# Kernel optimization log

Hardware: AMD Instinct MI355X
Metric: run time of the kernel (lower is better)

## Reference

```python
import jax, jax.numpy as jnp
import numpy as np

ALPHA = 1.0  # module hardcodes self.alpha = 1.0


def _normalize(m):
    # torch: diag(rowsum^-0.5) @ m @ diag(rowsum^-0.5) == broadcast row/col scaling
    r_inv = jnp.sum(m, axis=0) ** -0.5  # [V]
    return m * r_inv[:, None] * r_inv[None, :]


def setup_inputs() -> dict:
    key = jax.random.key(0)
    k1, k2, k3, k4 = jax.random.split(key, 4)
    V, D_IN, D_OUT, A, B = 2048, 64, 64, 8, 8
    adj = jax.random.uniform(k1, (V, V), dtype=jnp.float32)
    x = jax.random.normal(k2, (A, B, V, D_IN), dtype=jnp.float32)
    # xavier_normal_ on [D_IN, D_OUT]
    std = float(np.sqrt(2.0 / (D_IN + D_OUT)))
    weight = jax.random.normal(k3, (D_IN, D_OUT), dtype=jnp.float32) * std
    bias = jax.random.normal(k4, (D_OUT,), dtype=jnp.float32)
    return {"adj": adj, "x": x, "weight": weight, "bias": bias}


def reference(adj, x, weight, bias):
    # dropout is identity in eval mode
    adj_norm = _normalize(adj)
    sqr_norm = _normalize(adj @ adj)  # computed as in the original (alpha=1 zeroes it)
    m_norm = ALPHA * adj_norm + (1.0 - ALPHA) * sqr_norm  # [V, V]
    x_tmp = jnp.einsum('abvd,de->abve', x, weight)        # project features
    x_out = jnp.einsum('vj,abvd->abjd', m_norm, x_tmp)    # aggregate over nodes
    x_out = x_out + bias
    return jax.nn.relu(x_out)
```

## Files before the change

kernel.cpp:

```cpp
#include <hip/hip_runtime.h>
#include <cstddef>

typedef unsigned short u16;
typedef u16 u16x4 __attribute__((ext_vector_type(4)));
typedef u16 u16x8 __attribute__((ext_vector_type(8)));
typedef __bf16 bf16x8 __attribute__((ext_vector_type(8)));
typedef float f32x4 __attribute__((ext_vector_type(4)));

static constexpr int V  = 2048;
static constexpr int DD = 64;

__device__ __forceinline__ u16 f2b(float f) {
  union { float f; unsigned int i; } x; x.f = f;
  return (u16)((x.i + 0x7fffu + ((x.i >> 16) & 1u)) >> 16);
}

__device__ __forceinline__ void gll16(const void* g, void* l) {
  __builtin_amdgcn_global_load_lds(
      (const __attribute__((address_space(1))) void*)g,
      (__attribute__((address_space(3))) void*)l, 16, 0, 0);
}

__global__ __launch_bounds__(256) void k_pp(const float* __restrict__ adj,
                                            const float* __restrict__ x,
                                            const float* __restrict__ w,
                                            float* __restrict__ partial,
                                            u16* __restrict__ Yt) {
  __shared__ u16 WT[64 * 72];
  int t = threadIdx.x;
  int bid = blockIdx.x;

  if (bid < 256) {
    int rg = bid >> 3, cg = bid & 7;
    int col = cg * 256 + t;
    const float* p = adj + (size_t)(rg * 64) * V + col;
    float s = 0.f;
    for (int r = 0; r < 64; ++r) s += p[(size_t)r * V];
    partial[(size_t)rg * V + col] = s;
  } else {
    int pb = bid - 256;
    int ab = pb >> 4;
    int v0 = (pb & 15) * 128;

    {
      const float4* pw = (const float4*)(w + t * 16);
      float4 c0 = pw[0], c1 = pw[1], c2 = pw[2], c3 = pw[3];
      float vals[16] = {c0.x, c0.y, c0.z, c0.w, c1.x, c1.y, c1.z, c1.w,
                        c2.x, c2.y, c2.z, c2.w, c3.x, c3.y, c3.z, c3.w};
      #pragma unroll
      for (int k = 0; k < 16; ++k) {
        int idx = t * 16 + k;
        WT[(idx & 63) * 72 + (idx >> 6)] = f2b(vals[k]);
      }
    }
    __syncthreads();

    int lane = t & 63, wave = t >> 6;
    int q = lane >> 4, r = lane & 15;
    int vbase = v0 + wave * 32;

    bf16x8 a[4][2];
    #pragma unroll
    for (int i = 0; i < 4; ++i)
      #pragma unroll
      for (int kk = 0; kk < 2; ++kk)
        a[i][kk] = __builtin_bit_cast(bf16x8,
            *(const u16x8*)(WT + (i * 16 + r) * 72 + kk * 32 + q * 8));

    const f32x4 vzero = {0.f, 0.f, 0.f, 0.f};
    f32x4 acc[4][2];
    #pragma unroll
    for (int i = 0; i < 4; ++i) { acc[i][0] = vzero; acc[i][1] = vzero; }

    #pragma unroll
    for (int nt = 0; nt < 2; ++nt) {
      int v = vbase + nt * 16 + r;
      const float* xp = x + ((size_t)ab * V + v) * DD;
      #pragma unroll
      for (int kk = 0; kk < 2; ++kk) {
        const float4* p = (const float4*)(xp + kk * 32 + q * 8);
        float4 b0 = p[0], b1 = p[1];
        u16x8 bu;
        bu[0] = f2b(b0.x); bu[1] = f2b(b0.y); bu[2] = f2b(b0.z); bu[3] = f2b(b0.w);
        bu[4] = f2b(b1.x); bu[5] = f2b(b1.y); bu[6] = f2b(b1.z); bu[7] = f2b(b1.w);
        bf16x8 bf = __builtin_bit_cast(bf16x8, bu);
        #pragma unroll
        for (int i = 0; i < 4; ++i)
          acc[i][nt] = __builtin_amdgcn_mfma_f32_16x16x32_bf16(bf, a[i][kk], acc[i][nt], 0, 0, 0);
      }
    }

    #pragma unroll
    for (int i = 0; i < 4; ++i) {
      int e = ab * 64 + i * 16 + r;
      #pragma unroll
      for (int nt = 0; nt < 2; ++nt) {
        int v = vbase + nt * 16 + q * 4;
        u16x4 o;
        #pragma unroll
        for (int reg = 0; reg < 4; ++reg) o[reg] = f2b(acc[i][nt][reg]);
        *(u16x4*)(Yt + (size_t)e * V + v) = o;
      }
    }
  }
}

__global__ __launch_bounds__(256) void k_tn(const float* __restrict__ adj,
                                            const float* __restrict__ partial,
                                            u16* __restrict__ At) {
  __shared__ float T[64][65];
  __shared__ float rvv[64], rvj[64];
  int t = threadIdx.x;
  int bid = blockIdx.x;
  int v0 = (bid & 31) * 64;
  int j0 = (bid >> 5) * 64;

  if (t < 128) {
    int col = (t < 64) ? (v0 + t) : (j0 + (t - 64));
    float s = 0.f;
    #pragma unroll
    for (int i = 0; i < 32; ++i) s += partial[(size_t)i * V + col];
    float rv = rsqrtf(s);
    if (t < 64) rvv[t] = rv; else rvj[t - 64] = rv;
  }
  __syncthreads();
  #pragma unroll
  for (int it = 0; it < 2; ++it) {
    int f = t + it * 256;
    int row = f >> 3;
    int cc = (f & 7) * 8;
    float rv = rvv[row];
    const float4* p = (const float4*)(adj + (size_t)(v0 + row) * V + j0 + cc);
    float4 a0 = p[0], a1 = p[1];
    T[row][cc + 0] = a0.x * rv; T[row][cc + 1] = a0.y * rv;
    T[row][cc + 2] = a0.z * rv; T[row][cc + 3] = a0.w * rv;
    T[row][cc + 4] = a1.x * rv; T[row][cc + 5] = a1.y * rv;
    T[row][cc + 6] = a1.z * rv; T[row][cc + 7] = a1.w * rv;
  }
  __syncthreads();
  #pragma unroll
  for (int it = 0; it < 2; ++it) {
    int f = t + it * 256;
    int jr = f >> 3;
    int vc = (f & 7) * 8;
    float rj = rvj[jr];
    u16x8 o;
    #pragma unroll
    for (int k = 0; k < 8; ++k) o[k] = f2b(T[vc + k][jr] * rj);
    *(u16x8*)(At + (size_t)(j0 + jr) * V + v0 + vc) = o;
  }
}

static constexpr int ABUF  = 128 * 64;
static constexpr int BUFSZ = 2 * ABUF;

__global__ __launch_bounds__(256) void k_gemm(const u16* __restrict__ At,
                                              const u16* __restrict__ Yt,
                                              const float* __restrict__ bias,
                                              float* __restrict__ out) {
  __shared__ u16 lds[2 * BUFSZ];
  const int t = threadIdx.x;
  const int bid = blockIdx.x;
  const int swz = (bid & 7) * 64 + (bid >> 3);
  const int m0 = (swz & 15) * 128;
  const int n0 = (swz >> 4) * 128;
  const int lane = t & 63, wave = t >> 6;
  const int wm = (wave & 1) * 64;
  const int wn = (wave >> 1) * 64;
  const int q = lane >> 4, r = lane & 15;

  auto stage = [&](int base, int k0) {
    #pragma unroll
    for (int l = 0; l < 4; ++l) {
      int g = l * 256 + t;
      int row = g >> 3;
      int ch = (g & 7) ^ (row & 7);
      gll16(At + (size_t)(m0 + row) * V + k0 + ch * 8, (void*)(lds + base + g * 8));
      gll16(Yt + (size_t)(n0 + row) * V + k0 + ch * 8, (void*)(lds + base + ABUF + g * 8));
    }
  };

  const f32x4 vzero = {0.f, 0.f, 0.f, 0.f};
  f32x4 acc[4][4];
  #pragma unroll
  for (int i = 0; i < 4; ++i)
    #pragma unroll
    for (int j = 0; j < 4; ++j) acc[i][j] = vzero;

  stage(0, 0);
  asm volatile("s_waitcnt vmcnt(0)" ::: "memory");
  __builtin_amdgcn_s_barrier();

  int cb = 0;
  for (int tt = 0; tt < 32; ++tt) {
    const int nb = cb ^ BUFSZ;
    if (tt < 31) stage(nb, (tt + 1) * 64);
    __builtin_amdgcn_sched_barrier(0);

    #pragma unroll
    for (int kk = 0; kk < 2; ++kk) {
      bf16x8 a[4], b[4];
      #pragma unroll
      for (int i = 0; i < 4; ++i) {
        int row = wm + i * 16 + r;
        int c = (kk * 4 + q) ^ (row & 7);
        a[i] = __builtin_bit_cast(bf16x8,
            *(const u16x8*)(lds + cb + row * 64 + c * 8));
      }
      #pragma unroll
      for (int j = 0; j < 4; ++j) {
        int row = wn + j * 16 + r;
        int c = (kk * 4 + q) ^ (row & 7);
        b[j] = __builtin_bit_cast(bf16x8,
            *(const u16x8*)(lds + cb + ABUF + row * 64 + c * 8));
      }
      __builtin_amdgcn_s_setprio(1);
      #pragma unroll
      for (int i = 0; i < 4; ++i)
        #pragma unroll
        for (int j = 0; j < 4; ++j)
          acc[i][j] = __builtin_amdgcn_mfma_f32_16x16x32_bf16(
              a[i], b[j], acc[i][j], 0, 0, 0);
      __builtin_amdgcn_s_setprio(0);
    }

    asm volatile("s_waitcnt vmcnt(0)" ::: "memory");
    __builtin_amdgcn_s_barrier();
    cb = nb;
  }

  #pragma unroll
  for (int j = 0; j < 4; ++j) {
    int n = n0 + wn + j * 16 + r;
    int e = n & 63;
    int ab = n >> 6;
    float bv = bias[e];
    float* ob = out + (size_t)ab * (V * DD);
    #pragma unroll
    for (int i = 0; i < 4; ++i) {
      #pragma unroll
      for (int reg = 0; reg < 4; ++reg) {
        int jj = m0 + wm + i * 16 + q * 4 + reg;
        ob[(size_t)jj * DD + e] = fmaxf(acc[i][j][reg] + bv, 0.f);
      }
    }
  }
}

extern "C" void kernel_launch(void* const* d_in, const int* in_sizes, int n_in,
                              void* d_out, int out_size, void* d_ws, size_t ws_size,
                              hipStream_t stream) {
  const float* adj  = (const float*)d_in[0];
  const float* x    = (const float*)d_in[1];
  const float* w    = (const float*)d_in[2];
  const float* bias = (const float*)d_in[3];
  float* out = (float*)d_out;

  char* ws = (char*)d_ws;
  u16*   At      = (u16*)ws;
  u16*   Yt      = (u16*)(ws + ((size_t)8 << 20));
  float* partial = (float*)(ws + ((size_t)24 << 20));

  k_pp<<<1280, 256, 0, stream>>>(adj, x, w, partial, Yt);
  k_tn<<<1024, 256, 0, stream>>>(adj, partial, At);
  k_gemm<<<512, 256, 0, stream>>>(At, Yt, bias, out);
}
```

Before: 143.9 us.

## Fuse three kernels into one cooperative kernel with grid syncs

Merges the column-sum/projection, transpose-normalize and GEMM kernels into a single cooperative kernel of 512 blocks, separated by grid-wide barriers. Each block now handles two work items per phase, and the column-sum partials use 64 row groups of 32 rows. The aim is to remove two kernel launch boundaries and the tail idle time between them. In exchange it adds grid-sync cost and less parallelism in the early phases, and it depends on all 512 blocks being co-resident (launch_bounds 256,2).

```diff
diff --git a/kernel.cpp b/kernel.cpp
--- a/kernel.cpp
+++ b/kernel.cpp
@@ -1,5 +1,8 @@
 #include <hip/hip_runtime.h>
+#include <hip/hip_cooperative_groups.h>
 #include <cstddef>
+
+namespace cg = cooperative_groups;
 
 typedef unsigned short u16;
 typedef u16 u16x4 __attribute__((ext_vector_type(4)));
@@ -21,27 +24,31 @@
       (__attribute__((address_space(3))) void*)l, 16, 0, 0);
 }
 
-__global__ __launch_bounds__(256) void k_pp(const float* __restrict__ adj,
-                                            const float* __restrict__ x,
-                                            const float* __restrict__ w,
-                                            float* __restrict__ partial,
-                                            u16* __restrict__ Yt) {
-  __shared__ u16 WT[64 * 72];
-  int t = threadIdx.x;
-  int bid = blockIdx.x;
-
-  if (bid < 256) {
+static constexpr int ABUF  = 128 * 64;
+static constexpr int BUFSZ = 2 * ABUF;
+
+__global__ __launch_bounds__(256, 2) void k_mega(
+    const float* __restrict__ adj, const float* __restrict__ x,
+    const float* __restrict__ w, const float* __restrict__ bias,
+    float* __restrict__ partial, u16* __restrict__ At,
+    u16* __restrict__ Yt, float* __restrict__ out) {
+  __shared__ u16 lds[2 * BUFSZ];
+  const int t = threadIdx.x;
+  const int bid = blockIdx.x;
+  const int lane = t & 63, wave = t >> 6;
+  const int q = lane >> 4, r = lane & 15;
+
+  {
     int rg = bid >> 3, cg = bid & 7;
     int col = cg * 256 + t;
-    const float* p = adj + (size_t)(rg * 64) * V + col;
+    const float* p = adj + (size_t)(rg * 32) * V + col;
     float s = 0.f;
-    for (int r = 0; r < 64; ++r) s += p[(size_t)r * V];
+    for (int rr = 0; rr < 32; ++rr) s += p[(size_t)rr * V];
     partial[(size_t)rg * V + col] = s;
-  } else {
-    int pb = bid - 256;
-    int ab = pb >> 4;
-    int v0 = (pb & 15) * 128;
-
+  }
+
+  {
+    u16* WT = lds;
     {
       const float4* pw = (const float4*)(w + t * 16);
       float4 c0 = pw[0], c1 = pw[1], c2 = pw[2], c3 = pw[3];
@@ -55,10 +62,6 @@
     }
     __syncthreads();
 
-    int lane = t & 63, wave = t >> 6;
-    int q = lane >> 4, r = lane & 15;
-    int vbase = v0 + wave * 32;
-
     bf16x8 a[4][2];
     #pragma unroll
     for (int i = 0; i < 4; ++i)
@@ -68,180 +71,186 @@
             *(const u16x8*)(WT + (i * 16 + r) * 72 + kk * 32 + q * 8));
 
     const f32x4 vzero = {0.f, 0.f, 0.f, 0.f};
-    f32x4 acc[4][2];
-    #pragma unroll
-    for (int i = 0; i < 4; ++i) { acc[i][0] = vzero; acc[i][1] = vzero; }
-
-    #pragma unroll
-    for (int nt = 0; nt < 2; ++nt) {
-      int v = vbase + nt * 16 + r;
-      const float* xp = x + ((size_t)ab * V + v) * DD;
-      #pragma unroll
-      for (int kk = 0; kk < 2; ++kk) {
-        const float4* p = (const float4*)(xp + kk * 32 + q * 8);
-        float4 b0 = p[0], b1 = p[1];
-        u16x8 bu;
-        bu[0] = f2b(b0.x); bu[1] = f2b(b0.y); bu[2] = f2b(b0.z); bu[3] = f2b(b0.w);
-        bu[4] = f2b(b1.x); bu[5] = f2b(b1.y); bu[6] = f2b(b1.z); bu[7] = f2b(b1.w);
-        bf16x8 bf = __builtin_bit_cast(bf16x8, bu);
-        #pragma unroll
-        for (int i = 0; i < 4; ++i)
-          acc[i][nt] = __builtin_amdgcn_mfma_f32_16x16x32_bf16(bf, a[i][kk], acc[i][nt], 0, 0, 0);
-      }
-    }
-
-    #pragma unroll
-    for (int i = 0; i < 4; ++i) {
-      int e = ab * 64 + i * 16 + r;
+    #pragma unroll
+    for (int sub = 0; sub < 2; ++sub) {
+      int pb = bid * 2 + sub;
+      int ab = pb >> 4;
+      int v0 = (pb & 15) * 128;
+      int vbase = v0 + wave * 32;
+
+      f32x4 acc[4][2];
+      #pragma unroll
+      for (int i = 0; i < 4; ++i) { acc[i][0] = vzero; acc[i][1] = vzero; }
+
       #pragma unroll
       for (int nt = 0; nt < 2; ++nt) {
-        int v = vbase + nt * 16 + q * 4;
-        u16x4 o;
-        #pragma unroll
-        for (int reg = 0; reg < 4; ++reg) o[reg] = f2b(acc[i][nt][reg]);
-        *(u16x4*)(Yt + (size_t)e * V + v) = o;
-      }
-    }
-  }
-}
-
-__global__ __launch_bounds__(256) void k_tn(const float* __restrict__ adj,
-                                            const float* __restrict__ partial,
-                                            u16* __restrict__ At) {
-  __shared__ float T[64][65];
-  __shared__ float rvv[64], rvj[64];
-  int t = threadIdx.x;
-  int bid = blockIdx.x;
-  int v0 = (bid & 31) * 64;
-  int j0 = (bid >> 5) * 64;
-
-  if (t < 128) {
-    int col = (t < 64) ? (v0 + t) : (j0 + (t - 64));
-    float s = 0.f;
-    #pragma unroll
-    for (int i = 0; i < 32; ++i) s += partial[(size_t)i * V + col];
-    float rv = rsqrtf(s);
-    if (t < 64) rvv[t] = rv; else rvj[t - 64] = rv;
-  }
-  __syncthreads();
-  #pragma unroll
-  for (int it = 0; it < 2; ++it) {
-    int f = t + it * 256;
-    int row = f >> 3;
-    int cc = (f & 7) * 8;
-    float rv = rvv[row];
-    const float4* p = (const float4*)(adj + (size_t)(v0 + row) * V + j0 + cc);
-    float4 a0 = p[0], a1 = p[1];
-    T[row][cc + 0] = a0.x * rv; T[row][cc + 1] = a0.y * rv;
-    T[row][cc + 2] = a0.z * rv; T[row][cc + 3] = a0.w * rv;
-    T[row][cc + 4] = a1.x * rv; T[row][cc + 5] = a1.y * rv;
-    T[row][cc + 6] = a1.z * rv; T[row][cc + 7] = a1.w * rv;
-  }
-  __syncthreads();
-  #pragma unroll
-  for (int it = 0; it < 2; ++it) {
-    int f = t + it * 256;
-    int jr = f >> 3;
-    int vc = (f & 7) * 8;
-    float rj = rvj[jr];
-    u16x8 o;
-    #pragma unroll
-    for (int k = 0; k < 8; ++k) o[k] = f2b(T[vc + k][jr] * rj);
-    *(u16x8*)(At + (size_t)(j0 + jr) * V + v0 + vc) = o;
-  }
-}
-
-static constexpr int ABUF  = 128 * 64;
-static constexpr int BUFSZ = 2 * ABUF;
-
-__global__ __launch_bounds__(256) void k_gemm(const u16* __restrict__ At,
-                                              const u16* __restrict__ Yt,
-                                              const float* __restrict__ bias,
-                                              float* __restrict__ out) {
-  __shared__ u16 lds[2 * BUFSZ];
-  const int t = threadIdx.x;
-  const int bid = blockIdx.x;
-  const int swz = (bid & 7) * 64 + (bid >> 3);
-  const int m0 = (swz & 15) * 128;
-  const int n0 = (swz >> 4) * 128;
-  const int lane = t & 63, wave = t >> 6;
-  const int wm = (wave & 1) * 64;
-  const int wn = (wave >> 1) * 64;
-  const int q = lane >> 4, r = lane & 15;
-
-  auto stage = [&](int base, int k0) {
-    #pragma unroll
-    for (int l = 0; l < 4; ++l) {
-      int g = l * 256 + t;
-      int row = g >> 3;
-      int ch = (g & 7) ^ (row & 7);
-      gll16(At + (size_t)(m0 + row) * V + k0 + ch * 8, (void*)(lds + base + g * 8));
-      gll16(Yt + (size_t)(n0 + row) * V + k0 + ch * 8, (void*)(lds + base + ABUF + g * 8));
-    }
-  };
-
-  const f32x4 vzero = {0.f, 0.f, 0.f, 0.f};
-  f32x4 acc[4][4];
-  #pragma unroll
-  for (int i = 0; i < 4; ++i)
-    #pragma unroll
-    for (int j = 0; j < 4; ++j) acc[i][j] = vzero;
-
-  stage(0, 0);
-  asm volatile("s_waitcnt vmcnt(0)" ::: "memory");
-  __builtin_amdgcn_s_barrier();
-
-  int cb = 0;
-  for (int tt = 0; tt < 32; ++tt) {
-    const int nb = cb ^ BUFSZ;
-    if (tt < 31) stage(nb, (tt + 1) * 64);
-    __builtin_amdgcn_sched_barrier(0);
-
-    #pragma unroll
-    for (int kk = 0; kk < 2; ++kk) {
-      bf16x8 a[4], b[4];
+        int v = vbase + nt * 16 + r;
+        const float* xp = x + ((size_t)ab * V + v) * DD;
+        #pragma unroll
+        for (int kk = 0; kk < 2; ++kk) {
+          const float4* p = (const float4*)(xp + kk * 32 + q * 8);
+          float4 b0 = p[0], b1 = p[1];
+          u16x8 bu;
+          bu[0] = f2b(b0.x); bu[1] = f2b(b0.y); bu[2] = f2b(b0.z); bu[3] = f2b(b0.w);
+          bu[4] = f2b(b1.x); bu[5] = f2b(b1.y); bu[6] = f2b(b1.z); bu[7] = f2b(b1.w);
+          bf16x8 bf = __builtin_bit_cast(bf16x8, bu);
+          #pragma unroll
+          for (int i = 0; i < 4; ++i)
+            acc[i][nt] = __builtin_amdgcn_mfma_f32_16x16x32_bf16(bf, a[i][kk], acc[i][nt], 0, 0, 0);
+        }
+      }
+
       #pragma unroll
       for (int i = 0; i < 4; ++i) {
-        int row = wm + i * 16 + r;
-        int c = (kk * 4 + q) ^ (row & 7);
-        a[i] = __builtin_bit_cast(bf16x8,
-            *(const u16x8*)(lds + cb + row * 64 + c * 8));
-      }
-      #pragma unroll
-      for (int j = 0; j < 4; ++j) {
-        int row = wn + j * 16 + r;
-        int c = (kk * 4 + q) ^ (row & 7);
-        b[j] = __builtin_bit_cast(bf16x8,
-            *(const u16x8*)(lds + cb + ABUF + row * 64 + c * 8));
-      }
-      __builtin_amdgcn_s_setprio(1);
-      #pragma unroll
-      for (int i = 0; i < 4; ++i)
-        #pragma unroll
-        for (int j = 0; j < 4; ++j)
-          acc[i][j] = __builtin_amdgcn_mfma_f32_16x16x32_bf16(
-              a[i], b[j], acc[i][j], 0, 0, 0);
-      __builtin_amdgcn_s_setprio(0);
-    }
-
+        int e = ab * 64 + i * 16 + r;
+        #pragma unroll
+        for (int nt = 0; nt < 2; ++nt) {
+          int v = vbase + nt * 16 + q * 4;
+          u16x4 o;
+          #pragma unroll
+          for (int reg = 0; reg < 4; ++reg) o[reg] = f2b(acc[i][nt][reg]);
+          *(u16x4*)(Yt + (size_t)e * V + v) = o;
+        }
+      }
+    }
+  }
+
+  __threadfence();
+  cg::this_grid().sync();
+
+  {
+    float (*T)[65] = (float(*)[65])lds;
+    float* rvv = (float*)((char*)lds + 17408);
+    float* rvj = (float*)((char*)lds + 17664);
+
+    #pragma unroll
+    for (int sub = 0; sub < 2; ++sub) {
+      int tb = bid * 2 + sub;
+      int v0 = (tb & 31) * 64;
+      int j0 = (tb >> 5) * 64;
+
+      if (sub) __syncthreads();
+      if (t < 128) {
+        int col = (t < 64) ? (v0 + t) : (j0 + (t - 64));
+        float s = 0.f;
+        #pragma unroll
+        for (int i = 0; i < 64; ++i) s += partial[(size_t)i * V + col];
+        float rv = rsqrtf(s);
+        if (t < 64) rvv[t] = rv; else rvj[t - 64] = rv;
+      }
+      __syncthreads();
+      #pragma unroll
+      for (int it = 0; it < 2; ++it) {
+        int f = t + it * 256;
+        int row = f >> 3;
+        int cc = (f & 7) * 8;
+        float rv = rvv[row];
+        const float4* p = (const float4*)(adj + (size_t)(v0 + row) * V + j0 + cc);
+        float4 a0 = p[0], a1 = p[1];
+        T[row][cc + 0] = a0.x * rv; T[row][cc + 1] = a0.y * rv;
+        T[row][cc + 2] = a0.z * rv; T[row][cc + 3] = a0.w * rv;
+        T[row][cc + 4] = a1.x * rv; T[row][cc + 5] = a1.y * rv;
+        T[row][cc + 6] = a1.z * rv; T[row][cc + 7] = a1.w * rv;
+      }
+      __syncthreads();
+      #pragma unroll
+      for (int it = 0; it < 2; ++it) {
+        int f = t + it * 256;
+        int jr = f >> 3;
+        int vc = (f & 7) * 8;
+        float rj = rvj[jr];
+        u16x8 o;
+        #pragma unroll
+        for (int k = 0; k < 8; ++k) o[k] = f2b(T[vc + k][jr] * rj);
+        *(u16x8*)(At + (size_t)(j0 + jr) * V + v0 + vc) = o;
+      }
+    }
+  }
+
+  __threadfence();
+  cg::this_grid().sync();
+
+  {
+    const int swz = (bid & 7) * 64 + (bid >> 3);
+    const int m0 = (swz & 15) * 128;
+    const int n0 = (swz >> 4) * 128;
+    const int wm = (wave & 1) * 64;
+    const int wn = (wave >> 1) * 64;
+
+    auto stage = [&](int base, int k0) {
+      #pragma unroll
+      for (int l = 0; l < 4; ++l) {
+        int g = l * 256 + t;
+        int row = g >> 3;
+        int ch = (g & 7) ^ (row & 7);
+        gll16(At + (size_t)(m0 + row) * V + k0 + ch * 8, (void*)(lds + base + g * 8));
+        gll16(Yt + (size_t)(n0 + row) * V + k0 + ch * 8, (void*)(lds + base + ABUF + g * 8));
+      }
+    };
+
+    const f32x4 vzero = {0.f, 0.f, 0.f, 0.f};
+    f32x4 acc[4][4];
+    #pragma unroll
+    for (int i = 0; i < 4; ++i)
+      #pragma unroll
+      for (int j = 0; j < 4; ++j) acc[i][j] = vzero;
+
+    stage(0, 0);
     asm volatile("s_waitcnt vmcnt(0)" ::: "memory");
     __builtin_amdgcn_s_barrier();
-    cb = nb;
-  }
-
-  #pragma unroll
-  for (int j = 0; j < 4; ++j) {
-    int n = n0 + wn + j * 16 + r;
-    int e = n & 63;
-    int ab = n >> 6;
-    float bv = bias[e];
-    float* ob = out + (size_t)ab * (V * DD);
-    #pragma unroll
-    for (int i = 0; i < 4; ++i) {
-      #pragma unroll
-      for (int reg = 0; reg < 4; ++reg) {
-        int jj = m0 + wm + i * 16 + q * 4 + reg;
-        ob[(size_t)jj * DD + e] = fmaxf(acc[i][j][reg] + bv, 0.f);
+
+    int cb = 0;
+    for (int tt = 0; tt < 32; ++tt) {
+      const int nb = cb ^ BUFSZ;
+      if (tt < 31) stage(nb, (tt + 1) * 64);
+      __builtin_amdgcn_sched_barrier(0);
+
+      #pragma unroll
+      for (int kk = 0; kk < 2; ++kk) {
+        bf16x8 a[4], b[4];
+        #pragma unroll
+        for (int i = 0; i < 4; ++i) {
+          int row = wm + i * 16 + r;
+          int c = (kk * 4 + q) ^ (row & 7);
+          a[i] = __builtin_bit_cast(bf16x8,
+              *(const u16x8*)(lds + cb + row * 64 + c * 8));
+        }
+        #pragma unroll
+        for (int j = 0; j < 4; ++j) {
+          int row = wn + j * 16 + r;
+          int c = (kk * 4 + q) ^ (row & 7);
+          b[j] = __builtin_bit_cast(bf16x8,
+              *(const u16x8*)(lds + cb + ABUF + row * 64 + c * 8));
+        }
+        __builtin_amdgcn_s_setprio(1);
+        #pragma unroll
+        for (int i = 0; i < 4; ++i)
+          #pragma unroll
+          for (int j = 0; j < 4; ++j)
+            acc[i][j] = __builtin_amdgcn_mfma_f32_16x16x32_bf16(
+                a[i], b[j], acc[i][j], 0, 0, 0);
+        __builtin_amdgcn_s_setprio(0);
+      }
+
+      asm volatile("s_waitcnt vmcnt(0)" ::: "memory");
+      __builtin_amdgcn_s_barrier();
+      cb = nb;
+    }
+
+    #pragma unroll
+    for (int j = 0; j < 4; ++j) {
+      int n = n0 + wn + j * 16 + r;
+      int e = n & 63;
+      int ab = n >> 6;
+      float bv = bias[e];
+      float* ob = out + (size_t)ab * (V * DD);
+      #pragma unroll
+      for (int i = 0; i < 4; ++i) {
+        #pragma unroll
+        for (int reg = 0; reg < 4; ++reg) {
+          int jj = m0 + wm + i * 16 + q * 4 + reg;
+          ob[(size_t)jj * DD + e] = fmaxf(acc[i][j][reg] + bv, 0.f);
+        }
       }
     }
   }
@@ -261,7 +270,7 @@
   u16*   Yt      = (u16*)(ws + ((size_t)8 << 20));
   float* partial = (float*)(ws + ((size_t)24 << 20));
 
-  k_pp<<<1280, 256, 0, stream>>>(adj, x, w, partial, Yt);
-  k_tn<<<1024, 256, 0, stream>>>(adj, partial, At);
-  k_gemm<<<512, 256, 0, stream>>>(At, Yt, bias, out);
-}
+  void* args[] = {(void*)&adj, (void*)&x, (void*)&w, (void*)&bias,
+                  (void*)&partial, (void*)&At, (void*)&Yt, (void*)&out};
+  hipLaunchCooperativeKernel((void*)k_mega, dim3(512), dim3(256), args, 0, stream);
+}
```

Result: slower. 396.6 us (+175.7%).
